# Performance work log

Hardware: AMD Instinct MI355X
Metric: run time of the kernel (lower is better)

The kernel has to match this reference:

```python
import jax, jax.numpy as jnp
import numpy as np
from jax import lax

EPS = 1e-5

def setup_inputs() -> dict:
    key = jax.random.key(0)
    k1, k2, k3, k4, k5, k6 = jax.random.split(key, 6)
    x = jax.random.normal(k1, (1, 64, 31, 96, 96), dtype=jnp.float32)
    # small init scale keeps gate pre-activations in a sane range
    w = jax.random.normal(k2, (256, 64, 3, 3, 3), dtype=jnp.float32) * 0.05
    gamma = jax.random.uniform(k3, (256,), dtype=jnp.float32)
    beta = jax.random.normal(k4, (256,), dtype=jnp.float32) * 0.1
    mean = jax.random.normal(k5, (256,), dtype=jnp.float32) * 0.1
    var = jax.random.uniform(k6, (256,), dtype=jnp.float32) + 0.5
    return {"x": x, "w": w, "gamma": gamma, "beta": beta, "mean": mean, "var": var}

def _bcast(p):
    return p[None, :, None, None, None]

def reference(x, w, gamma, beta, mean, var):
    # Conv3d (bias=False), stride 1, padding 1, NCDHW
    gates = lax.conv_general_dilated(
        x, w, window_strides=(1, 1, 1), padding=[(1, 1)] * 3,
        dimension_numbers=("NCDHW", "OIDHW", "NCDHW"))
    # BatchNorm3d (inference, running stats)
    scale = gamma * lax.rsqrt(var + EPS)
    gates = gates * _bcast(scale) + _bcast(beta - mean * scale)
    C = 64  # out_channels
    Wx = jnp.tanh(gates[:, 0 * C:1 * C])
    ft = jax.nn.sigmoid(gates[:, 1 * C:2 * C])
    rt = jax.nn.sigmoid(gates[:, 2 * C:3 * C])
    X = jnp.tanh(gates[:, 3 * C:4 * C])  # act == 'tanh'
    # time axis (dim 2) to front: (D, B, C, H, W)
    Wt = jnp.moveaxis(Wx, 2, 0)
    Ft = jnp.moveaxis(ft, 2, 0)
    Rt = jnp.moveaxis(rt, 2, 0)
    Xt = jnp.moveaxis(X, 2, 0)
    # t = 0: Ct = 1 - ft (note: Wx unused at first step, per source)
    C0 = 1.0 - Ft[0]
    h0 = Rt[0] * C0 + (1.0 - Rt[0]) * Xt[0]
    def step(Ct, inp):
        wx, f, r, xx = inp
        Ct = f * Ct + (1.0 - f) * wx
        ht = r * Ct + (1.0 - r) * xx
        return Ct, ht
    _, hs = lax.scan(step, C0, (Wt[1:], Ft[1:], Rt[1:], Xt[1:]))
    hts = jnp.concatenate([h0[None], hs], axis=0)  # (D,B,C,H,W)
    return jnp.moveaxis(hts, 0, 2)  # (B,C,D,H,W)
```

## Files before the change

### kernel.cpp

```cpp
#include <hip/hip_runtime.h>
#include <cstddef>

#define CI_  64
#define CO_  256
#define DD_  31
#define HH_  96
#define WW_  96
#define HW_  (HH_*WW_)
#define DHW_ (DD_*HW_)
#define EPSV 1e-5f

#define PD_   33
#define PH_   98
#define PW_   98
#define PHW_  9604
#define PDHW_ 316932

#define S_COL 8
#define S_CIG 144
#define S_ROW 1152
#define S_DD  11520
#define NTASK 4320
#define NTASKP 4352
#define XH_N  (NTASKP*8)

#define NTILE 72
#define NBLK  (NTILE*DD_)

#define GBLK 32768
#define GDSTR ((size_t)NTILE * GBLK)

#define PREP_RB 216
#define PREP_PB 1239
#define PREP_TB 279
#define PREP_NB (PREP_RB + PREP_PB + PREP_TB)

typedef _Float16 half8   __attribute__((ext_vector_type(8)));
typedef _Float16 half4v  __attribute__((ext_vector_type(4)));
typedef float    float4v __attribute__((ext_vector_type(4)));

__device__ __forceinline__ void gl_lds16(const _Float16* g, _Float16* l) {
  __builtin_amdgcn_global_load_lds(
      (const __attribute__((address_space(1))) unsigned int*)(g),
      (__attribute__((address_space(3))) unsigned int*)(l), 16, 0, 0);
}

__global__ __launch_bounds__(256) void prep_k(const float* __restrict__ w,
                                              const float* __restrict__ x,
                                              _Float16* __restrict__ wr2,
                                              _Float16* __restrict__ xt) {
  const int bid = blockIdx.x;
  if (bid < PREP_RB) {
    int idx = bid * 256 + threadIdx.x;
    int lw   = idx & 15;
    int quad = (idx >> 4) & 3;
    int cog  = (idx >> 6) & 15;
    int tkc  = idx >> 10;
    int kc   = tkc & 1;
    int t    = tkc >> 1;
    int co   = cog * 16 + lw;
    int cib  = kc * 32 + quad * 8;
    half8 v;
#pragma unroll
    for (int s = 0; s < 8; s++)
      v[s] = (_Float16)w[(size_t)co * 1728 + (size_t)(cib + s) * 27 + t];
    *(half8*)(wr2 + (size_t)idx * 8) = v;
  } else if (bid < PREP_RB + PREP_PB) {
    int p = (bid - PREP_RB) * 256 + threadIdx.x;
    if (p >= PDHW_) return;
    int pd  = p / PHW_;
    int rem = p - pd * PHW_;
    int ph  = rem / PW_;
    int pw  = rem - ph * PW_;
    bool in = (pd >= 1) & (pd <= DD_) & (ph >= 1) & (ph <= HH_) & (pw >= 1) & (pw <= WW_);
    if (in) return;
    half8 z = (half8)(_Float16)0.f;
#pragma unroll
    for (int cig = 0; cig < 8; cig++)
      *(half8*)(xt + ((size_t)cig * PDHW_ + p) * 8) = z;
  } else {
    int idx = (bid - PREP_RB - PREP_PB) * 256 + threadIdx.x;
    if (idx >= 31 * 96 * 24) return;
    int wq  = idx % 24;
    int rem = idx / 24;
    int h   = rem % 96;
    int d   = rem / 96;
    const float* xp = x + (size_t)d * HW_ + (size_t)h * WW_ + wq * 4;
    size_t p0 = (size_t)(d + 1) * PHW_ + (size_t)(h + 1) * PW_ + (wq * 4 + 1);
#pragma unroll 1
    for (int cig = 0; cig < 8; cig++) {
      float4 vv[8];
#pragma unroll
      for (int s = 0; s < 8; s++)
        vv[s] = *(const float4*)(xp + (size_t)(cig * 8 + s) * DHW_);
#pragma unroll
      for (int k = 0; k < 4; k++) {
        half8 o;
#pragma unroll
        for (int s = 0; s < 8; s++) o[s] = (_Float16)(&vv[s].x)[k];
        *(half8*)(xt + ((size_t)cig * PDHW_ + p0 + k) * 8) = o;
      }
    }
  }
}

__device__ __forceinline__ float tanh_f(float v) {
  float t = __expf(-2.f * fabsf(v));
  return copysignf((1.f - t) * __builtin_amdgcn_rcpf(1.f + t), v);
}
__device__ __forceinline__ float sigm_f(float v) {
  return __builtin_amdgcn_rcpf(1.f + __expf(-v));
}

__global__ __launch_bounds__(512, 4) void conv_mfma_k(
    const _Float16* __restrict__ xt, const _Float16* __restrict__ wr2,
    const float* __restrict__ gamma, const float* __restrict__ beta,
    const float* __restrict__ mean, const float* __restrict__ var,
    _Float16* __restrict__ gates)
{
  __shared__ _Float16 xh[XH_N];

  const int bid  = blockIdx.x;
  const int flat = (bid & 7) * 279 + (bid >> 3);
  const int d    = flat / NTILE;
  const int bx   = flat - d * NTILE;
  const int wti  = bx % 6;
  const int hti  = bx / 6;
  const int h0   = hti * 8, w0 = wti * 16;

  const int tid  = threadIdx.x;
  const int lane = tid & 63;
  const int wave = __builtin_amdgcn_readfirstlane(tid >> 6);
  const int wm   = wave >> 2;
  const int wn   = wave & 3;
  const int lw   = lane & 15;
  const int quad = lane >> 4;

#pragma unroll 1
  for (int it = 0; it < 9; ++it) {
    const int wb = it * 512 + wave * 64;
    if (wb < NTASKP) {
      const int task = wb + lane;
      const int tt   = task < NTASK ? task : (NTASK - 1);
      int col = tt % 18;
      int rc  = tt / 18;
      int cig = rc & 7;
      int dr  = rc >> 3;
      int dd  = dr / 10;
      int row = dr - dd * 10;
      const _Float16* g = xt + (((size_t)cig * PDHW_ + (size_t)(d + dd) * PHW_ +
                                 (size_t)(h0 + row) * PW_ + (w0 + col)) << 3);
      gl_lds16(g, xh + (size_t)wb * 8);
    }
  }

  float4v acc[4][4];
#pragma unroll
  for (int m = 0; m < 4; m++)
#pragma unroll
    for (int j = 0; j < 4; j++) acc[m][j] = (float4v)0.f;

  __syncthreads();

  const int abase0 = quad * S_CIG + lw * S_COL + (wm * 4) * S_ROW;
  half8 af[6];
  half8 bf[4];
#pragma unroll
  for (int kd = 0; kd < 3; ++kd) {
#pragma unroll
    for (int kc = 0; kc < 2; ++kc) {
#pragma unroll
      for (int kw = 0; kw < 3; ++kw) {
        const int ab = abase0 + kd * S_DD + kc * (4 * S_CIG) + kw * S_COL;
#pragma unroll
        for (int r = 0; r < 6; ++r)
          af[r] = *(const half8*)(xh + ab + r * S_ROW);
#pragma unroll
        for (int kh = 0; kh < 3; ++kh) {
          const int t = (kd * 3 + kh) * 3 + kw;
          const _Float16* bp =
              wr2 + (((size_t)((t * 2 + kc) * 16 + wn * 4)) << 9) + (lane << 3);
#pragma unroll
          for (int j = 0; j < 4; ++j)
            bf[j] = *(const half8*)(bp + ((size_t)j << 9));
          __builtin_amdgcn_s_setprio(1);
#pragma unroll
          for (int j = 0; j < 4; ++j) {
            acc[0][j] = __builtin_amdgcn_mfma_f32_16x16x32_f16(af[kh    ], bf[j], acc[0][j], 0, 0, 0);
            acc[1][j] = __builtin_amdgcn_mfma_f32_16x16x32_f16(af[kh + 1], bf[j], acc[1][j], 0, 0, 0);
            acc[2][j] = __builtin_amdgcn_mfma_f32_16x16x32_f16(af[kh + 2], bf[j], acc[2][j], 0, 0, 0);
            acc[3][j] = __builtin_amdgcn_mfma_f32_16x16x32_f16(af[kh + 3], bf[j], acc[3][j], 0, 0, 0);
          }
          __builtin_amdgcn_s_setprio(0);
        }
      }
    }
  }

  _Float16* gb = gates + (size_t)(d * NTILE + bx) * GBLK + wn * 4;
  const bool istanh = (wn == 0) || (wn == 3);
#pragma unroll
  for (int j = 0; j < 4; j++) {
    const int co = wn * 64 + j * 16 + lw;
    const int c  = j * 16 + lw;
    const float s  = gamma[co] * rsqrtf(var[co] + EPSV);
    const float bb = fmaf(-mean[co], s, beta[co]);
#pragma unroll
    for (int m = 0; m < 4; m++) {
      half4v hv;
#pragma unroll
      for (int reg = 0; reg < 4; reg++) {
        float v = fmaf(acc[m][j][reg], s, bb);
        hv[reg] = (_Float16)(istanh ? tanh_f(v) : sigm_f(v));
      }
      const int q = (wm * 4 + m) * 4 + quad;
      *(half4v*)(gb + (size_t)c * 512 + q * 16) = hv;
    }
  }
}

__global__ __launch_bounds__(256) void recurrence_k(const _Float16* __restrict__ gates,
                                                    float* __restrict__ out) {
  const int idx = blockIdx.x * 256 + threadIdx.x;
  const int q   = idx & 31;
  const int t2  = idx >> 5;
  const int c   = t2 / NTILE;
  const int bx  = t2 - c * NTILE;
  const int hti = bx / 6, wti = bx - hti * 6;
  const int sp  = q * 4;
  const int h   = hti * 8 + (sp >> 4);
  const int w   = wti * 16 + (sp & 15);

  const _Float16* g0 = gates + (size_t)bx * GBLK + (size_t)c * 512 + q * 16;
  float* op = out + (size_t)c * DHW_ + (size_t)h * WW_ + w;

#define LDLO(dv) (*(const half8*)(g0 + (size_t)(dv) * GDSTR))
#define LDHI(dv) (*(const half8*)(g0 + (size_t)(dv) * GDSTR + 8))

  half8 clo = LDLO(0), chi = LDHI(0);
  half8 nlo = LDLO(1), nhi = LDHI(1);
  float C[4];
  {
    float4 st;
#pragma unroll
    for (int k = 0; k < 4; k++) {
      C[k] = 1.f - (float)clo[4 + k];
      float r0 = (float)chi[k], x0 = (float)chi[4 + k];
      (&st.x)[k] = fmaf(r0, C[k] - x0, x0);
    }
    *(float4*)op = st;
  }
#pragma unroll 1
  for (int d = 1; d < DD_; d++) {
    clo = nlo; chi = nhi;
    if (d < DD_ - 1) {
      nlo = LDLO(d + 1); nhi = LDHI(d + 1);
    }
    float4 st;
#pragma unroll
    for (int k = 0; k < 4; k++) {
      float wx0 = (float)clo[k],     f0 = (float)clo[4 + k];
      float r0  = (float)chi[k],     x0 = (float)chi[4 + k];
      C[k] = fmaf(f0, C[k] - wx0, wx0);
      (&st.x)[k] = fmaf(r0, C[k] - x0, x0);
    }
    *(float4*)(op + (size_t)d * HW_) = st;
  }
#undef LDLO
#undef LDHI
}

extern "C" void kernel_launch(void* const* d_in, const int* in_sizes, int n_in,
                              void* d_out, int out_size, void* d_ws, size_t ws_size,
                              hipStream_t stream) {
  const float* x     = (const float*)d_in[0];
  const float* w     = (const float*)d_in[1];
  const float* gamma = (const float*)d_in[2];
  const float* beta  = (const float*)d_in[3];
  const float* mean  = (const float*)d_in[4];
  const float* var   = (const float*)d_in[5];
  float* out = (float*)d_out;

  _Float16* wr2   = (_Float16*)d_ws;
  _Float16* xt    = (_Float16*)((char*)d_ws + 884736);
  _Float16* gates = (_Float16*)((char*)d_ws + 884736 + 40567296);

  prep_k<<<PREP_NB, 256, 0, stream>>>(w, x, wr2, xt);
  conv_mfma_k<<<NBLK, 512, 0, stream>>>(xt, wr2, gamma, beta, mean, var, gates);
  recurrence_k<<<(64 * NTILE * 32) / 256, 256, 0, stream>>>(gates, out);
}
```

Before: 412.6 us.

## Stage gate epilogue through swizzled LDS and interleave gates per pixel for recurrence

```diff
diff --git a/kernel.cpp b/kernel.cpp
--- a/kernel.cpp
+++ b/kernel.cpp
@@ -197,7 +197,8 @@
     }
   }
 
-  _Float16* gb = gates + (size_t)(d * NTILE + bx) * GBLK + wn * 4;
+  __syncthreads();
+
   const bool istanh = (wn == 0) || (wn == 3);
 #pragma unroll
   for (int j = 0; j < 4; j++) {
@@ -205,69 +206,61 @@
     const int c  = j * 16 + lw;
     const float s  = gamma[co] * rsqrtf(var[co] + EPSV);
     const float bb = fmaf(-mean[co], s, beta[co]);
+    const int cbase = c << 10;
+    const int key   = (c & 7) << 4;
 #pragma unroll
     for (int m = 0; m < 4; m++) {
-      half4v hv;
 #pragma unroll
       for (int reg = 0; reg < 4; reg++) {
         float v = fmaf(acc[m][j][reg], s, bb);
-        hv[reg] = (_Float16)(istanh ? tanh_f(v) : sigm_f(v));
+        _Float16 a = (_Float16)(istanh ? tanh_f(v) : sigm_f(v));
+        const int sp = wm * 64 + m * 16 + quad * 4 + reg;
+        *(_Float16*)((char*)xh + cbase + (((sp << 3) + (wn << 1)) ^ key)) = a;
       }
-      const int q = (wm * 4 + m) * 4 + quad;
-      *(half4v*)(gb + (size_t)c * 512 + q * 16) = hv;
-    }
+    }
+  }
+  __syncthreads();
+
+  _Float16* gb = gates + (size_t)(d * NTILE + bx) * GBLK;
+#pragma unroll
+  for (int r = 0; r < 8; r++) {
+    const int c = wave * 8 + r;
+    const half8 rv = *(const half8*)((const char*)xh + (c << 10) +
+                                     ((lane ^ (c & 7)) << 4));
+    *(half8*)(gb + (size_t)c * 512 + lane * 8) = rv;
   }
 }
 
 __global__ __launch_bounds__(256) void recurrence_k(const _Float16* __restrict__ gates,
                                                     float* __restrict__ out) {
   const int idx = blockIdx.x * 256 + threadIdx.x;
-  const int q   = idx & 31;
-  const int t2  = idx >> 5;
+  const int sp  = idx & 127;
+  const int t2  = idx >> 7;
   const int c   = t2 / NTILE;
   const int bx  = t2 - c * NTILE;
   const int hti = bx / 6, wti = bx - hti * 6;
-  const int sp  = q * 4;
   const int h   = hti * 8 + (sp >> 4);
   const int w   = wti * 16 + (sp & 15);
 
-  const _Float16* g0 = gates + (size_t)bx * GBLK + (size_t)c * 512 + q * 16;
+  const _Float16* g0 = gates + (size_t)bx * GBLK + (size_t)c * 512 + sp * 4;
   float* op = out + (size_t)c * DHW_ + (size_t)h * WW_ + w;
 
-#define LDLO(dv) (*(const half8*)(g0 + (size_t)(dv) * GDSTR))
-#define LDHI(dv) (*(const half8*)(g0 + (size_t)(dv) * GDSTR + 8))
-
-  half8 clo = LDLO(0), chi = LDHI(0);
-  half8 nlo = LDLO(1), nhi = LDHI(1);
-  float C[4];
-  {
-    float4 st;
-#pragma unroll
-    for (int k = 0; k < 4; k++) {
-      C[k] = 1.f - (float)clo[4 + k];
-      float r0 = (float)chi[k], x0 = (float)chi[4 + k];
-      (&st.x)[k] = fmaf(r0, C[k] - x0, x0);
-    }
-    *(float4*)op = st;
-  }
-#pragma unroll 1
-  for (int d = 1; d < DD_; d++) {
-    clo = nlo; chi = nhi;
-    if (d < DD_ - 1) {
-      nlo = LDLO(d + 1); nhi = LDHI(d + 1);
-    }
-    float4 st;
-#pragma unroll
-    for (int k = 0; k < 4; k++) {
-      float wx0 = (float)clo[k],     f0 = (float)clo[4 + k];
-      float r0  = (float)chi[k],     x0 = (float)chi[4 + k];
-      C[k] = fmaf(f0, C[k] - wx0, wx0);
-      (&st.x)[k] = fmaf(r0, C[k] - x0, x0);
-    }
-    *(float4*)(op + (size_t)d * HW_) = st;
-  }
-#undef LDLO
-#undef LDHI
+#define LD(dv) (*(const half4v*)(g0 + (size_t)(dv) * GDSTR))
+  half4v p[4];
+#pragma unroll
+  for (int i = 0; i < 4; i++) p[i] = LD(i);
+
+  float C = 0.f;
+#pragma unroll
+  for (int d = 0; d < DD_; d++) {
+    half4v cur = p[d & 3];
+    if (d + 4 < DD_) p[d & 3] = LD(d + 4);
+    float wx = (float)cur[0], f = (float)cur[1];
+    float r  = (float)cur[2], x = (float)cur[3];
+    C = (d == 0) ? (1.f - f) : fmaf(f, C - wx, wx);
+    op[(size_t)d * HW_] = fmaf(r, C - x, x);
+  }
+#undef LD
 }
 
 extern "C" void kernel_launch(void* const* d_in, const int* in_sizes, int n_in,
@@ -287,5 +280,5 @@
 
   prep_k<<<PREP_NB, 256, 0, stream>>>(w, x, wr2, xt);
   conv_mfma_k<<<NBLK, 512, 0, stream>>>(xt, wr2, gamma, beta, mean, var, gates);
-  recurrence_k<<<(64 * NTILE * 32) / 256, 256, 0, stream>>>(gates, out);
-}
+  recurrence_k<<<(64 * NTILE * 128) / 256, 256, 0, stream>>>(gates, out);
+}
```

New measurement: 406.8 us. Within noise of the previous version (-1.4%).
